# Performance work log

Hardware: AMD Instinct MI355X
Metric: run time of the kernel (lower is better)

Reference implementation:

```python
import jax, jax.numpy as jnp
import numpy as np

DIM = 1024

def setup_inputs() -> dict:
    key = jax.random.key(0)
    k1, k2 = jax.random.split(key)
    X = jax.random.normal(k1, (4, 4096, DIM), dtype=jnp.float32)
    # nn.Linear(dim, 3*dim): weight [3*dim, dim], bias [3*dim]
    W = jax.random.normal(k2, (3 * DIM, DIM), dtype=jnp.float32) * (1.0 / np.sqrt(DIM))
    b = jnp.zeros((3 * DIM,), dtype=jnp.float32)
    return {"X": X, "W": W, "b": b}

def reference(X, W, b):
    dim = X.shape[-1]
    # fused QKV projection: [B,S,3D]
    QKV = jnp.einsum('bsd,ed->bse', X, W) + b
    Q, K, V = jnp.split(QKV, 3, axis=-1)
    scale = 1.0 / jnp.sqrt(jnp.asarray(dim, X.dtype))
    scores = jnp.einsum('bqd,bkd->bqk', Q, K) * scale  # [B,S,S]
    attn = jax.nn.softmax(scores, axis=-1)
    return jnp.einsum('bqk,bkd->bqd', attn, V)
```

## Files before the change

### kernel.cpp

```cpp
#include <hip/hip_runtime.h>
#include <cstdint>

typedef unsigned short u16;
typedef __attribute__((ext_vector_type(8))) short bf16x8;
typedef __attribute__((ext_vector_type(4))) float f32x4;

#define DIM   1024
#define BATCH 4
#define SEQ   4096
#define E3    3072
#define MTOT  (BATCH*SEQ)

__device__ __forceinline__ u16 f2bf(float x) {
    union { float f; unsigned u; } v; v.f = x;
    unsigned r = v.u + 0x7FFFu + ((v.u >> 16) & 1u);
    return (u16)(r >> 16);
}

__device__ __forceinline__ void gl16(const void* g, void* l) {
    __builtin_amdgcn_global_load_lds(
        (const __attribute__((address_space(1))) void*)g,
        (__attribute__((address_space(3))) void*)l, 16, 0, 0);
}

__device__ __forceinline__ void gemm256(
    const u16* __restrict__ A, int sA,
    const u16* __restrict__ B, int sB,
    int K, int m0, int n0,
    u16* lds, f32x4 acc[8][4])
{
    const int tid = threadIdx.x;
    const int w   = tid >> 6, L = tid & 63;
    const int rL  = L & 15, kq = L >> 4;
    const int wg8 = (w>>2)*8;
    const int jb4 = 4*(w&3);

    const int mA = wg8 + (w&3);
    const size_t gA  = (size_t)(m0 + mA*16 + rL)*sA + kq*8;
    const size_t gAm = (size_t)64*sA;
    const size_t gB0 = (size_t)(n0 + (2*w)*16 + rL)*sB + kq*8;
    const size_t gB1 = gB0 + (size_t)16*sB;

    const int ldsA  = (mA*2)*512 + L*8;
    const int ldsB0 = 16384 + (2*w*2)*512 + L*8;
    const int ldsB1 = 16384 + ((2*w+1)*2)*512 + L*8;

    const int NT = K >> 6;
    bf16x8 av[4], bv[4];

#define FEN    __builtin_amdgcn_sched_barrier(0)
#define BARR   __builtin_amdgcn_s_barrier()
#define VMW(n) asm volatile("s_waitcnt vmcnt(" #n ")")

#define SAU(mh, tn) { u16* bn = lds + (((tn)&1)<<15); \
    const size_t g = gA + (size_t)(mh)*gAm + (size_t)(tn)*64; \
    gl16(A + g,      bn + ldsA + (mh)*4096); \
    gl16(A + g + 32, bn + ldsA + (mh)*4096 + 512); }

#define SBU(ks, tn) { u16* bn = lds + (((tn)&1)<<15); \
    const size_t g = (size_t)(tn)*64 + (size_t)(ks)*32; \
    gl16(B + gB0 + g, bn + ldsB0 + (ks)*512); \
    gl16(B + gB1 + g, bn + ldsB1 + (ks)*512); }

#define RD(mh, ks, tcur) { const u16* bc = lds + (((tcur)&1)<<15); \
    _Pragma("unroll") \
    for (int i = 0; i < 4; ++i) \
        av[i] = *(const bf16x8*)&bc[((wg8+(mh)*4+i)*2+(ks))*512 + L*8]; \
    if ((mh) == 0) { \
        _Pragma("unroll") \
        for (int j = 0; j < 4; ++j) \
            bv[j] = *(const bf16x8*)&bc[16384 + ((jb4+j)*2+(ks))*512 + L*8]; } }

#define MM(mh) { \
    __builtin_amdgcn_s_setprio(1); \
    _Pragma("unroll") \
    for (int i = 0; i < 4; ++i) \
        _Pragma("unroll") \
        for (int j = 0; j < 4; ++j) \
            acc[(mh)*4+i][j] = __builtin_amdgcn_mfma_f32_16x16x32_bf16(av[i], bv[j], acc[(mh)*4+i][j], 0,0,0); \
    __builtin_amdgcn_s_setprio(0); }

    SAU(0,0); SBU(0,0); SAU(1,0); SBU(1,0);

    for (int tt = 0; tt < NT-1; ++tt) {
        FEN; VMW(4); BARR; FEN;
        RD(0,0,tt); FEN; SAU(0,tt+1); FEN; MM(0);
        FEN; VMW(4); BARR; FEN;
        RD(1,0,tt); FEN; SBU(0,tt+1); FEN; MM(1);
        FEN; VMW(4); BARR; FEN;
        RD(0,1,tt); FEN; SAU(1,tt+1); FEN; MM(0);
        FEN;
        RD(1,1,tt); FEN; SBU(1,tt+1); FEN; MM(1);
    }
    {   const int tt = NT-1;
        FEN; VMW(4); BARR; FEN; RD(0,0,tt); FEN; MM(0);
        FEN; VMW(2); BARR; FEN; RD(1,0,tt); FEN; MM(1);
        FEN; VMW(0); BARR; FEN; RD(0,1,tt); FEN; MM(0);
        FEN;                    RD(1,1,tt); FEN; MM(1);
    }

#undef SAU
#undef SBU
#undef RD
#undef MM
#undef FEN
#undef BARR
#undef VMW
}

__global__ __launch_bounds__(256)
void cvt_bf16(const float* __restrict__ x, u16* __restrict__ y) {
    size_t i = ((size_t)blockIdx.x*256 + threadIdx.x)*4;
    float4 v = *(const float4*)&x[i];
    ushort4 h;
    h.x = f2bf(v.x); h.y = f2bf(v.y); h.z = f2bf(v.z); h.w = f2bf(v.w);
    *(ushort4*)&y[i] = h;
}

__global__ __launch_bounds__(512,2)
void gemm_qkv(const u16* __restrict__ Xbf, const u16* __restrict__ Wbf,
              const float* __restrict__ bias,
              u16* __restrict__ Qh, u16* __restrict__ Kh,
              u16* __restrict__ Vth)
{
    __shared__ __align__(16) u16 lds[65536];
    f32x4 acc[8][4];
    #pragma unroll
    for (int i=0;i<8;++i)
        #pragma unroll
        for (int j=0;j<4;++j) acc[i][j] = (f32x4){0.f,0.f,0.f,0.f};

    const int F = blockIdx.y*12 + blockIdx.x;
    const int c = F & 7, s = F >> 3;
    const int mrow = c*8 + (s & 7);
    const int ncol = s >> 3;
    const int m0 = mrow*256, n0 = ncol*256;
    gemm256(Xbf, DIM, Wbf, DIM, DIM, m0, n0, lds, acc);

    const int t = threadIdx.x, w = t>>6, L = t&63;
    const int wm = 128*(w>>2), wn = 64*(w&3);
    const int cl = L&15, rq = (L>>4)*4;
    const int region = n0 >> 10;
    const float qscale = 0.03125f;

    if (region < 2) {
        u16* Dst = region ? Kh : Qh;
        const float fs = region ? 1.0f : qscale;
        #pragma unroll
        for (int j = 0; j < 4; ++j) {
            float bc = bias[n0 + wn + j*16 + cl];
            #pragma unroll
            for (int i = 0; i < 8; ++i)
                #pragma unroll
                for (int r = 0; r < 4; ++r)
                    acc[i][j][r] = (acc[i][j][r] + bc)*fs;
        }
        const int d0 = (n0 & 1023) + wn;
        #pragma unroll
        for (int p = 0; p < 2; ++p) {
            const int nt0 = 2*p, nt1 = 2*p+1;
            #pragma unroll
            for (int i = 0; i < 8; ++i) {
                int row0 = m0 + wm + i*16 + rq;
                int bi = row0 >> 12, s0 = row0 & (SEQ-1);
                #pragma unroll
                for (int r = 0; r < 4; ++r) {
                    float v0 = acc[i][nt0][r], v1 = acc[i][nt1][r];
                    float x0 = __shfl_xor(v0, 1, 64);
                    float x1 = __shfl_xor(v1, 1, 64);
                    unsigned wv; int colb;
                    if ((cl & 1) == 0) {
                        wv   = (unsigned)f2bf(v0) | ((unsigned)f2bf(x0) << 16);
                        colb = nt0*16 + cl;
                    } else {
                        wv   = (unsigned)f2bf(x1) | ((unsigned)f2bf(v1) << 16);
                        colb = nt1*16 + (cl-1);
                    }
                    size_t idx = ((size_t)bi*SEQ + s0 + r)*DIM + d0 + colb;
                    *(unsigned*)&Dst[idx] = wv;
                }
            }
        }
    } else {
        #pragma unroll
        for (int j = 0; j < 4; ++j) {
            int col = n0 + wn + j*16 + cl;
            float bc = bias[col];
            int d = col & (DIM-1);
            #pragma unroll
            for (int i = 0; i < 8; ++i) {
                int row0 = m0 + wm + i*16 + rq;
                int bi = row0 >> 12, s0 = row0 & (SEQ-1);
                ushort4 hv;
                hv.x = f2bf(acc[i][j][0] + bc);
                hv.y = f2bf(acc[i][j][1] + bc);
                hv.z = f2bf(acc[i][j][2] + bc);
                hv.w = f2bf(acc[i][j][3] + bc);
                size_t base = ((size_t)bi*DIM + d)*SEQ + s0;
                *(ushort4*)&Vth[base] = hv;
            }
        }
    }
}

__global__ __launch_bounds__(512,2)
void gemm_scores(const u16* __restrict__ Qh, const u16* __restrict__ Kh,
                 u16* __restrict__ S0, u16* __restrict__ S1,
                 u16* __restrict__ S2, u16* __restrict__ S3)
{
    __shared__ __align__(16) u16 lds[65536];
    f32x4 acc[8][4];
    #pragma unroll
    for (int i=0;i<8;++i)
        #pragma unroll
        for (int j=0;j<4;++j) acc[i][j] = (f32x4){0.f,0.f,0.f,0.f};

    const int F = (blockIdx.z*16 + blockIdx.y)*16 + blockIdx.x;
    const int c = F & 7, s = F >> 3;
    const int st = s >> 5, v = s & 31;
    const int bz   = c >> 1;
    const int mrow = (c&1)*8 + (st>>1)*4 + (v>>3);
    const int ncol = (st&1)*8 + (v&7);
    const size_t qo = (size_t)bz*SEQ*DIM;
    const int m0 = mrow*256, n0 = ncol*256;
    gemm256(Qh + qo, DIM, Kh + qo, DIM, DIM, m0, n0, lds, acc);

    u16* Sb = (bz == 0) ? S0 : (bz == 1) ? S1 : (bz == 2) ? S2 : S3;
    const int t = threadIdx.x, w = t>>6, L = t&63;
    const int wm = 128*(w>>2), wn = 64*(w&3);
    const int cl = L&15, rq = (L>>4)*4;
    #pragma unroll
    for (int p = 0; p < 2; ++p) {
        const int nt0 = 2*p, nt1 = 2*p+1;
        #pragma unroll
        for (int i = 0; i < 8; ++i) {
            int row0 = m0 + wm + i*16 + rq;
            #pragma unroll
            for (int r = 0; r < 4; ++r) {
                float v0 = acc[i][nt0][r], v1 = acc[i][nt1][r];
                float x0 = __shfl_xor(v0, 1, 64);
                float x1 = __shfl_xor(v1, 1, 64);
                unsigned wv; int colb;
                if ((cl & 1) == 0) {
                    wv   = (unsigned)f2bf(v0) | ((unsigned)f2bf(x0) << 16);
                    colb = nt0*16 + cl;
                } else {
                    wv   = (unsigned)f2bf(x1) | ((unsigned)f2bf(v1) << 16);
                    colb = nt1*16 + (cl-1);
                }
                *(unsigned*)&Sb[(size_t)(row0 + r)*SEQ + n0 + wn + colb] = wv;
            }
        }
    }
}

__global__ __launch_bounds__(256)
void softmax_pack(u16* __restrict__ S0, u16* __restrict__ S1,
                  u16* __restrict__ S2, u16* __restrict__ S3)
{
    __shared__ float red[4];
    const int t = threadIdx.x, L = t & 63, w = t >> 6;
    const int gr = blockIdx.x, bz = gr >> 12, rr = gr & (SEQ-1);
    u16* Sb = (bz == 0) ? S0 : (bz == 1) ? S1 : (bz == 2) ? S2 : S3;
    u16* row = Sb + (size_t)rr*SEQ;

    float v[16];
    float m = -1e30f;
    #pragma unroll
    for (int j = 0; j < 2; ++j) {
        ushort4 x0 = *(const ushort4*)&row[t*8 + j*2048];
        ushort4 x1 = *(const ushort4*)&row[t*8 + j*2048 + 4];
        union { unsigned u; float f; } c;
        c.u = (unsigned)x0.x << 16; v[8*j+0] = c.f;
        c.u = (unsigned)x0.y << 16; v[8*j+1] = c.f;
        c.u = (unsigned)x0.z << 16; v[8*j+2] = c.f;
        c.u = (unsigned)x0.w << 16; v[8*j+3] = c.f;
        c.u = (unsigned)x1.x << 16; v[8*j+4] = c.f;
        c.u = (unsigned)x1.y << 16; v[8*j+5] = c.f;
        c.u = (unsigned)x1.z << 16; v[8*j+6] = c.f;
        c.u = (unsigned)x1.w << 16; v[8*j+7] = c.f;
    }
    #pragma unroll
    for (int i = 0; i < 16; ++i) m = fmaxf(m, v[i]);
    #pragma unroll
    for (int off = 32; off; off >>= 1) m = fmaxf(m, __shfl_xor(m, off, 64));
    if (L == 0) red[w] = m;
    __syncthreads();
    m = fmaxf(fmaxf(red[0],red[1]), fmaxf(red[2],red[3]));

    float s = 0.f;
    #pragma unroll
    for (int i = 0; i < 16; ++i) { v[i] = __expf(v[i] - m); s += v[i]; }
    #pragma unroll
    for (int off = 32; off; off >>= 1) s += __shfl_xor(s, off, 64);
    __syncthreads();
    if (L == 0) red[w] = s;
    __syncthreads();
    s = red[0]+red[1]+red[2]+red[3];
    const float inv = 1.0f / s;

    #pragma unroll
    for (int j = 0; j < 2; ++j) {
        ushort4 h0, h1;
        h0.x = f2bf(v[8*j+0]*inv); h0.y = f2bf(v[8*j+1]*inv);
        h0.z = f2bf(v[8*j+2]*inv); h0.w = f2bf(v[8*j+3]*inv);
        h1.x = f2bf(v[8*j+4]*inv); h1.y = f2bf(v[8*j+5]*inv);
        h1.z = f2bf(v[8*j+6]*inv); h1.w = f2bf(v[8*j+7]*inv);
        *(ushort4*)&row[t*8 + j*2048]     = h0;
        *(ushort4*)&row[t*8 + j*2048 + 4] = h1;
    }
}

__global__ __launch_bounds__(512,2)
void gemm_pv(const u16* __restrict__ P0, const u16* __restrict__ P1,
             const u16* __restrict__ P2, const u16* __restrict__ P3,
             const u16* __restrict__ Vth,
             float* __restrict__ O0, float* __restrict__ O1,
             float* __restrict__ O2, float* __restrict__ O3)
{
    __shared__ __align__(16) u16 lds[65536];
    f32x4 acc[8][4];
    #pragma unroll
    for (int i=0;i<8;++i)
        #pragma unroll
        for (int j=0;j<4;++j) acc[i][j] = (f32x4){0.f,0.f,0.f,0.f};

    const int F = (blockIdx.z*16 + blockIdx.y)*4 + blockIdx.x;
    const int c = F & 7, s = F >> 3;
    const int bz   = c >> 1;
    const int mrow = (c&1)*8 + (s>>2);
    const int ncol = s & 3;
    const u16* Pb = (bz == 0) ? P0 : (bz == 1) ? P1 : (bz == 2) ? P2 : P3;
    float*     Ob = (bz == 0) ? O0 : (bz == 1) ? O1 : (bz == 2) ? O2 : O3;
    const int m0 = mrow*256, n0 = ncol*256;
    gemm256(Pb, SEQ, Vth + (size_t)bz*DIM*SEQ, SEQ, SEQ, m0, n0, lds, acc);

    const int t = threadIdx.x, w = t>>6, L = t&63;
    const int wm = 128*(w>>2), wn = 64*(w&3);
    const int cl = L&15, rq = (L>>4)*4;
    #pragma unroll
    for (int j = 0; j < 4; ++j) {
        int col = n0 + wn + j*16 + cl;
        #pragma unroll
        for (int i = 0; i < 8; ++i) {
            int row0 = m0 + wm + i*16 + rq;
            #pragma unroll
            for (int r = 0; r < 4; ++r)
                Ob[(size_t)(row0 + r)*DIM + col] = acc[i][j][r];
        }
    }
}

__global__ __launch_bounds__(256)
void copy_out(const float* __restrict__ src, float* __restrict__ dst)
{
    size_t i = ((size_t)blockIdx.x*256 + threadIdx.x)*4;
    *(float4*)&dst[i] = *(const float4*)&src[i];
}

extern "C" void kernel_launch(void* const* d_in, const int* in_sizes, int n_in,
                              void* d_out, int out_size, void* d_ws, size_t ws_size,
                              hipStream_t stream) {
    const float* X    = (const float*)d_in[0];
    const float* W    = (const float*)d_in[1];
    const float* bias = (const float*)d_in[2];
    float* out = (float*)d_out;

    const size_t MB = (size_t)1 << 20;
    if (ws_size < 192*MB) return;
    char* ws = (char*)d_ws;
    char* wo = (char*)d_out;
    u16* Qh  = (u16*)ws;
    u16* Kh  = (u16*)(ws + 32*MB);
    u16* Vth = (u16*)(ws + 64*MB);
    u16* S0  = (u16*)(ws + 96*MB);
    u16* S1  = (u16*)(ws + 128*MB);
    u16* S2  = (u16*)(ws + 160*MB);
    u16* Xbf = (u16*)wo;
    u16* Wbf = (u16*)(wo + 32*MB);
    u16* S3  = (u16*)(wo + 32*MB);
    float* O0 = (float*)wo;
    float* O1 = (float*)(wo + 16*MB);
    float* O2 = (float*)ws;
    float* O3 = (float*)(ws + 16*MB);

    cvt_bf16<<<MTOT*DIM/1024, 256, 0, stream>>>(X, Xbf);
    cvt_bf16<<<E3*DIM/1024,   256, 0, stream>>>(W, Wbf);

    gemm_qkv<<<dim3(E3/256, MTOT/256), 512, 0, stream>>>(
        Xbf, Wbf, bias, Qh, Kh, Vth);

    gemm_scores<<<dim3(SEQ/256, SEQ/256, BATCH), 512, 0, stream>>>(
        Qh, Kh, S0, S1, S2, S3);

    softmax_pack<<<MTOT, 256, 0, stream>>>(S0, S1, S2, S3);

    gemm_pv<<<dim3(DIM/256, SEQ/256, BATCH), 512, 0, stream>>>(
        S0, S1, S2, S3, Vth, O0, O1, O2, O3);

    copy_out<<<(32*MB/sizeof(float))/1024, 256, 0, stream>>>(
        (const float*)ws, out + 8*MB);
}
```

Before: 561.9 us.

## Restructure GEMM LDS staging with XOR-swizzled row-major tiles and simpler pipeline

Rewrites the shared 256x256 GEMM tile loader so each wave loads 32 full rows of A and B with an XOR-swizzled k offset into LDS, replacing the earlier fragment-interleaved layout. The fine-grained four-phase schedule, which interleaved loads with MFMA groups under priority hints, becomes one double-buffered stage per k-tile with two barriers and a vmcnt wait. The goal is fewer bank conflicts and simpler code for the compiler to schedule. The cost is coarser overlap between global loads and compute, and the s_setprio hints are gone.

```diff
diff --git a/kernel.cpp b/kernel.cpp
--- a/kernel.cpp
+++ b/kernel.cpp
@@ -35,74 +35,79 @@
     const int wg8 = (w>>2)*8;
     const int jb4 = 4*(w&3);
 
-    const int mA = wg8 + (w&3);
-    const size_t gA  = (size_t)(m0 + mA*16 + rL)*sA + kq*8;
-    const size_t gAm = (size_t)64*sA;
-    const size_t gB0 = (size_t)(n0 + (2*w)*16 + rL)*sB + kq*8;
-    const size_t gB1 = gB0 + (size_t)16*sB;
-
-    const int ldsA  = (mA*2)*512 + L*8;
-    const int ldsB0 = 16384 + (2*w*2)*512 + L*8;
-    const int ldsB1 = 16384 + ((2*w+1)*2)*512 + L*8;
+    const int lr    = L >> 3;
+    const int kperm = ((L & 7) ^ lr) * 8;
+    const size_t gA0 = (size_t)(m0 + w*32 + lr) * sA + kperm;
+    const size_t gB0 = (size_t)(n0 + w*32 + lr) * sB + kperm;
+    const int dA = w*2048;
+    const int dB = 16384 + w*2048;
+
+    const int rdr = rL * 64;
+    const int kp0 = ((0 + kq) ^ (rL & 7)) * 8;
+    const int kp1 = ((4 + kq) ^ (rL & 7)) * 8;
 
     const int NT = K >> 6;
-    bf16x8 av[4], bv[4];
 
 #define FEN    __builtin_amdgcn_sched_barrier(0)
 #define BARR   __builtin_amdgcn_s_barrier()
 #define VMW(n) asm volatile("s_waitcnt vmcnt(" #n ")")
 
-#define SAU(mh, tn) { u16* bn = lds + (((tn)&1)<<15); \
-    const size_t g = gA + (size_t)(mh)*gAm + (size_t)(tn)*64; \
-    gl16(A + g,      bn + ldsA + (mh)*4096); \
-    gl16(A + g + 32, bn + ldsA + (mh)*4096 + 512); }
-
-#define SBU(ks, tn) { u16* bn = lds + (((tn)&1)<<15); \
-    const size_t g = (size_t)(tn)*64 + (size_t)(ks)*32; \
-    gl16(B + gB0 + g, bn + ldsB0 + (ks)*512); \
-    gl16(B + gB1 + g, bn + ldsB1 + (ks)*512); }
-
-#define RD(mh, ks, tcur) { const u16* bc = lds + (((tcur)&1)<<15); \
-    _Pragma("unroll") \
-    for (int i = 0; i < 4; ++i) \
-        av[i] = *(const bf16x8*)&bc[((wg8+(mh)*4+i)*2+(ks))*512 + L*8]; \
-    if ((mh) == 0) { \
-        _Pragma("unroll") \
-        for (int j = 0; j < 4; ++j) \
-            bv[j] = *(const bf16x8*)&bc[16384 + ((jb4+j)*2+(ks))*512 + L*8]; } }
-
-#define MM(mh) { \
-    __builtin_amdgcn_s_setprio(1); \
-    _Pragma("unroll") \
-    for (int i = 0; i < 4; ++i) \
-        _Pragma("unroll") \
-        for (int j = 0; j < 4; ++j) \
-            acc[(mh)*4+i][j] = __builtin_amdgcn_mfma_f32_16x16x32_bf16(av[i], bv[j], acc[(mh)*4+i][j], 0,0,0); \
-    __builtin_amdgcn_s_setprio(0); }
-
-    SAU(0,0); SBU(0,0); SAU(1,0); SBU(1,0);
-
-    for (int tt = 0; tt < NT-1; ++tt) {
-        FEN; VMW(4); BARR; FEN;
-        RD(0,0,tt); FEN; SAU(0,tt+1); FEN; MM(0);
-        FEN; VMW(4); BARR; FEN;
-        RD(1,0,tt); FEN; SBU(0,tt+1); FEN; MM(1);
-        FEN; VMW(4); BARR; FEN;
-        RD(0,1,tt); FEN; SAU(1,tt+1); FEN; MM(0);
-        FEN;
-        RD(1,1,tt); FEN; SBU(1,tt+1); FEN; MM(1);
-    }
-    {   const int tt = NT-1;
-        FEN; VMW(4); BARR; FEN; RD(0,0,tt); FEN; MM(0);
-        FEN; VMW(2); BARR; FEN; RD(1,0,tt); FEN; MM(1);
-        FEN; VMW(0); BARR; FEN; RD(0,1,tt); FEN; MM(0);
-        FEN;                    RD(1,1,tt); FEN; MM(1);
-    }
-
-#undef SAU
-#undef SBU
-#undef RD
-#undef MM
+#define STAGE8(tn) { u16* bb = lds + (((tn)&1)<<15); \
+    const size_t kk = (size_t)(tn)*64; \
+    gl16(A + gA0 + kk,                 bb + dA); \
+    gl16(A + gA0 + (size_t) 8*sA + kk, bb + dA + 512); \
+    gl16(A + gA0 + (size_t)16*sA + kk, bb + dA + 1024); \
+    gl16(A + gA0 + (size_t)24*sA + kk, bb + dA + 1536); \
+    gl16(B + gB0 + kk,                 bb + dB); \
+    gl16(B + gB0 + (size_t) 8*sB + kk, bb + dB + 512); \
+    gl16(B + gB0 + (size_t)16*sB + kk, bb + dB + 1024); \
+    gl16(B + gB0 + (size_t)24*sB + kk, bb + dB + 1536); }
+
+#define MFMA(a,b,c) __builtin_amdgcn_mfma_f32_16x16x32_bf16(a,b,c,0,0,0)
+
+    STAGE8(0);
+
+    for (int tt = 0; tt < NT; ++tt) {
+        BARR;
+        if (tt+1 < NT) { STAGE8(tt+1); FEN; VMW(8); }
+        else           { FEN; VMW(0); }
+        FEN; BARR; FEN;
+
+        const u16* bc = lds + ((tt&1)<<15);
+        bf16x8 av[4], bv[4];
+
+        #pragma unroll
+        for (int i=0;i<4;++i) av[i] = *(const bf16x8*)&bc[(wg8+i)*1024 + rdr + kp0];
+        #pragma unroll
+        for (int j=0;j<4;++j) bv[j] = *(const bf16x8*)&bc[16384 + (jb4+j)*1024 + rdr + kp0];
+        #pragma unroll
+        for (int i=0;i<4;++i)
+            #pragma unroll
+            for (int j=0;j<4;++j) acc[i][j] = MFMA(av[i], bv[j], acc[i][j]);
+        #pragma unroll
+        for (int i=0;i<4;++i) av[i] = *(const bf16x8*)&bc[(wg8+4+i)*1024 + rdr + kp0];
+        #pragma unroll
+        for (int i=0;i<4;++i)
+            #pragma unroll
+            for (int j=0;j<4;++j) acc[4+i][j] = MFMA(av[i], bv[j], acc[4+i][j]);
+        #pragma unroll
+        for (int i=0;i<4;++i) av[i] = *(const bf16x8*)&bc[(wg8+i)*1024 + rdr + kp1];
+        #pragma unroll
+        for (int j=0;j<4;++j) bv[j] = *(const bf16x8*)&bc[16384 + (jb4+j)*1024 + rdr + kp1];
+        #pragma unroll
+        for (int i=0;i<4;++i)
+            #pragma unroll
+            for (int j=0;j<4;++j) acc[i][j] = MFMA(av[i], bv[j], acc[i][j]);
+        #pragma unroll
+        for (int i=0;i<4;++i) av[i] = *(const bf16x8*)&bc[(wg8+4+i)*1024 + rdr + kp1];
+        #pragma unroll
+        for (int i=0;i<4;++i)
+            #pragma unroll
+            for (int j=0;j<4;++j) acc[4+i][j] = MFMA(av[i], bv[j], acc[4+i][j]);
+    }
+
+#undef STAGE8
+#undef MFMA
 #undef FEN
 #undef BARR
 #undef VMW
```

Result: faster. 524.4 us (-6.7%).
